# Optimization experiments

Measured on AMD Instinct MI355X. Metric: run time of the kernel, lower is better.

## Reference

```python
import jax, jax.numpy as jnp
import numpy as np

COST_CLASS = 1.0
COST_BBOX = 1.0
COST_GIOU = 1.0
ALPHA = 0.25
GAMMA = 2.0
EPS = 1e-8


def to_corners(b):
    # cxcywh -> xyxy
    cx, cy, w, h = b[..., 0], b[..., 1], b[..., 2], b[..., 3]
    return jnp.stack([cx - 0.5 * w, cy - 0.5 * h, cx + 0.5 * w, cy + 0.5 * h], axis=-1)


def generalized_iou(boxes1, boxes2):
    # boxes1: [N,4] xyxy, boxes2: [M,4] xyxy -> pairwise GIoU [N,M]
    area1 = (boxes1[:, 2] - boxes1[:, 0]) * (boxes1[:, 3] - boxes1[:, 1])  # [N]
    area2 = (boxes2[:, 2] - boxes2[:, 0]) * (boxes2[:, 3] - boxes2[:, 1])  # [M]
    lt = jnp.maximum(boxes1[:, None, :2], boxes2[None, :, :2])  # [N,M,2]
    rb = jnp.minimum(boxes1[:, None, 2:], boxes2[None, :, 2:])  # [N,M,2]
    wh = jnp.clip(rb - lt, 0.0)
    inter = wh[..., 0] * wh[..., 1]  # [N,M]
    union = area1[:, None] + area2[None, :] - inter
    iou = inter / (union + EPS)
    # smallest enclosing box
    lt_e = jnp.minimum(boxes1[:, None, :2], boxes2[None, :, :2])
    rb_e = jnp.maximum(boxes1[:, None, 2:], boxes2[None, :, 2:])
    wh_e = jnp.clip(rb_e - lt_e, 0.0)
    area_e = wh_e[..., 0] * wh_e[..., 1]
    return iou - (area_e - union) / (area_e + EPS)


def setup_inputs() -> dict:
    key = jax.random.key(0)
    k1, k2, k3, k4 = jax.random.split(key, 4)
    B, Q, C, T = 16, 900, 4, 1600
    logits = jax.random.normal(k1, (B, Q, C), dtype=jnp.float32)
    pred_bbox = jax.random.uniform(k2, (B, Q, 4), dtype=jnp.float32)
    target_bbox = jax.random.uniform(k3, (T, 4), dtype=jnp.float32)
    target_labels = jax.random.randint(k4, (T,), 0, C, dtype=jnp.int64)
    return {"logits": logits, "pred_bbox": pred_bbox,
            "target_bbox": target_bbox, "target_labels": target_labels}


def reference(logits, pred_bbox, target_bbox, target_labels):
    B, Q, C = logits.shape
    out_conf = jax.nn.sigmoid(logits.reshape(B * Q, C))  # [BQ, C]
    out_bbox = pred_bbox.reshape(B * Q, 4)
    # sigmoid focal classification cost
    neg_cost = (1.0 - ALPHA) * out_conf ** GAMMA * (-jnp.log(1.0 - out_conf + EPS))
    pos_cost = ALPHA * (1.0 - out_conf) ** GAMMA * (-jnp.log(out_conf + EPS))
    cost_class = pos_cost[:, target_labels] - neg_cost[:, target_labels]  # [BQ, T]
    # L1 cdist
    cost_bbox = jnp.sum(jnp.abs(out_bbox[:, None, :] - target_bbox[None, :, :]), axis=-1)  # [BQ, T]
    # pairwise GIoU cost
    cost_giou = -generalized_iou(to_corners(out_bbox), to_corners(target_bbox))  # [BQ, T]
    cost = COST_BBOX * cost_bbox + COST_CLASS * cost_class + COST_GIOU * cost_giou
    return cost.reshape(B, Q, -1)  # [B, Q, total_T]
```

## Files before the change

### kernel.cpp

```cpp
#include <hip/hip_runtime.h>
#include <hip/hip_bf16.h>
#include <math.h>

#define ALPHA 0.25f
#define EPS 1e-8f

__global__ __launch_bounds__(256) void class_cost_kernel(
    const float* __restrict__ logits,
    float* __restrict__ cc,
    int n)
{
    int i = blockIdx.x * 256 + threadIdx.x;
    if (i >= n) return;
    float x = logits[i];
    float p = 1.0f / (1.0f + expf(-x));
    float om = 1.0f - p;
    float pos = ALPHA * om * om * (-logf(p + EPS));
    float neg = (1.0f - ALPHA) * p * p * (-logf(om + EPS));
    cc[i] = pos - neg + 1.0f;
}

#define BQ_TILE 16

__global__ __launch_bounds__(256) void cost_kernel(
    const float* __restrict__ pred_bbox,
    const float* __restrict__ tgt_bbox,
    const int*   __restrict__ labels,
    const float* __restrict__ cc,
    float* __restrict__ out,
    int BQ, int T)
{
    int tg = blockIdx.x * 256 + threadIdx.x;
    int t0 = tg * 4;
    if (t0 >= T) return;
    int bq0 = blockIdx.y * BQ_TILE;

    float4 tb[4];
    float tx0[4], ty0[4], tx1[4], ty1[4], a2e[4];
    int lab[4];
    int4 lv = reinterpret_cast<const int4*>(labels)[tg];
    lab[0] = lv.x; lab[1] = lv.y; lab[2] = lv.z; lab[3] = lv.w;
    #pragma unroll
    for (int j = 0; j < 4; ++j) {
        tb[j] = reinterpret_cast<const float4*>(tgt_bbox)[t0 + j];
        tx0[j] = tb[j].x - 0.5f * tb[j].z;
        ty0[j] = tb[j].y - 0.5f * tb[j].w;
        tx1[j] = tb[j].x + 0.5f * tb[j].z;
        ty1[j] = tb[j].y + 0.5f * tb[j].w;
        a2e[j] = tb[j].z * tb[j].w + EPS;
    }

    #pragma unroll
    for (int i = 0; i < BQ_TILE; ++i) {
        int bq = bq0 + i;
        if (bq >= BQ) break;
        float4 pb = reinterpret_cast<const float4*>(pred_bbox)[bq];
        float4 cv = reinterpret_cast<const float4*>(cc)[bq];

        float px0 = pb.x - 0.5f * pb.z;
        float py0 = pb.y - 0.5f * pb.w;
        float px1 = pb.x + 0.5f * pb.z;
        float py1 = pb.y + 0.5f * pb.w;
        float area1 = pb.z * pb.w;

        float r[4];
        #pragma unroll
        for (int j = 0; j < 4; ++j) {
            float cls = (lab[j] == 0) ? cv.x : (lab[j] == 1) ? cv.y
                       : (lab[j] == 2) ? cv.z : cv.w;

            float l1 = (fabsf(pb.x - tb[j].x) + fabsf(pb.y - tb[j].y))
                     + (fabsf(pb.z - tb[j].z) + fabsf(pb.w - tb[j].w));

            float iwr = fminf(px1, tx1[j]) - fmaxf(px0, tx0[j]);
            float ihr = fminf(py1, ty1[j]) - fmaxf(py0, ty0[j]);
            float iw = fmaxf(iwr, 0.0f);
            float ih = fmaxf(ihr, 0.0f);
            float inter = iw * ih;

            float ew = (pb.z + tb[j].z) - iwr;
            float eh = (pb.w + tb[j].w) - ihr;
            float ae = fmaf(ew, eh, EPS);

            float u = (area1 + a2e[j]) - inter;

            float num = fmaf(inter, ae, u * u);
            float den = u * ae;
            float q = num * __builtin_amdgcn_rcpf(den);

            r[j] = (l1 + cls) - q;
        }
        float4 o = make_float4(r[0], r[1], r[2], r[3]);
        reinterpret_cast<float4*>(&out[(size_t)bq * T + t0])[0] = o;
    }
}

extern "C" void kernel_launch(void* const* d_in, const int* in_sizes, int n_in,
                              void* d_out, int out_size, void* d_ws, size_t ws_size,
                              hipStream_t stream) {
    const float* logits    = (const float*)d_in[0];
    const float* pred_bbox = (const float*)d_in[1];
    const float* tgt_bbox  = (const float*)d_in[2];
    const int*   labels    = (const int*)d_in[3];

    int BQ = in_sizes[1] / 4;
    int T  = in_sizes[3];

    float* cc = (float*)d_ws;

    int n_cc = in_sizes[0];
    class_cost_kernel<<<(n_cc + 255) / 256, 256, 0, stream>>>(logits, cc, n_cc);

    int tgroups = T / 4;
    dim3 grid((tgroups + 255) / 256, (BQ + BQ_TILE - 1) / BQ_TILE);
    cost_kernel<<<grid, 256, 0, stream>>>(pred_bbox, tgt_bbox, labels, cc,
                                          (float*)d_out, BQ, T);
}
```

Measured before the change: 124.7 us.

## Pack per-wave work units to eliminate idle lanes and precompute predicted corners

```diff
diff --git a/kernel.cpp b/kernel.cpp
--- a/kernel.cpp
+++ b/kernel.cpp
@@ -4,42 +4,66 @@
 
 #define ALPHA 0.25f
 #define EPS 1e-8f
+#define BQ_TILE 16
 
-__global__ __launch_bounds__(256) void class_cost_kernel(
+__global__ __launch_bounds__(256) void prep_kernel(
     const float* __restrict__ logits,
+    const float* __restrict__ pred_bbox,
     float* __restrict__ cc,
-    int n)
+    float4* __restrict__ pcorn,
+    int n_cc, int BQ)
 {
     int i = blockIdx.x * 256 + threadIdx.x;
-    if (i >= n) return;
-    float x = logits[i];
-    float p = 1.0f / (1.0f + expf(-x));
-    float om = 1.0f - p;
-    float pos = ALPHA * om * om * (-logf(p + EPS));
-    float neg = (1.0f - ALPHA) * p * p * (-logf(om + EPS));
-    cc[i] = pos - neg + 1.0f;
+    if (i < n_cc) {
+        float x = logits[i];
+        float p = 1.0f / (1.0f + expf(-x));
+        float om = 1.0f - p;
+        float pos = ALPHA * om * om * (-logf(p + EPS));
+        float neg = (1.0f - ALPHA) * p * p * (-logf(om + EPS));
+        cc[i] = pos - neg + 1.0f;
+    }
+    if (i < BQ) {
+        float4 pb = reinterpret_cast<const float4*>(pred_bbox)[i];
+        float4 c;
+        c.x = pb.x - 0.5f * pb.z;
+        c.y = pb.y - 0.5f * pb.w;
+        c.z = pb.x + 0.5f * pb.z;
+        c.w = pb.y + 0.5f * pb.w;
+        pcorn[i] = c;
+    }
 }
-
-#define BQ_TILE 16
 
 __global__ __launch_bounds__(256) void cost_kernel(
     const float* __restrict__ pred_bbox,
+    const float4* __restrict__ pcorn,
     const float* __restrict__ tgt_bbox,
     const int*   __restrict__ labels,
     const float* __restrict__ cc,
     float* __restrict__ out,
-    int BQ, int T)
+    int BQ, int T, int nTC, int nWU)
 {
-    int tg = blockIdx.x * 256 + threadIdx.x;
+    __shared__ float s_cc[4 * BQ_TILE * 4];
+
+    int wslot = threadIdx.x >> 6;
+    int lane  = threadIdx.x & 63;
+    int wu = blockIdx.x * 4 + wslot;
+    if (wu >= nWU) return;
+    int tc  = wu % nTC;
+    int bqt = wu / nTC;
+    int bq0 = bqt * BQ_TILE;
+
+    s_cc[wslot * 64 + lane] = cc[bq0 * 4 + lane];
+
+    int tg = tc * 64 + lane;
+    int TG = T >> 2;
+    if (tg >= TG) return;
     int t0 = tg * 4;
-    if (t0 >= T) return;
-    int bq0 = blockIdx.y * BQ_TILE;
 
     float4 tb[4];
     float tx0[4], ty0[4], tx1[4], ty1[4], a2e[4];
-    int lab[4];
+    int lidx[4];
     int4 lv = reinterpret_cast<const int4*>(labels)[tg];
-    lab[0] = lv.x; lab[1] = lv.y; lab[2] = lv.z; lab[3] = lv.w;
+    int lbl[4] = {lv.x, lv.y, lv.z, lv.w};
     #pragma unroll
     for (int j = 0; j < 4; ++j) {
         tb[j] = reinterpret_cast<const float4*>(tgt_bbox)[t0 + j];
@@ -48,32 +72,26 @@
         tx1[j] = tb[j].x + 0.5f * tb[j].z;
         ty1[j] = tb[j].y + 0.5f * tb[j].w;
         a2e[j] = tb[j].z * tb[j].w + EPS;
+        lidx[j] = wslot * 64 + lbl[j];
     }
 
     #pragma unroll
     for (int i = 0; i < BQ_TILE; ++i) {
         int bq = bq0 + i;
-        if (bq >= BQ) break;
         float4 pb = reinterpret_cast<const float4*>(pred_bbox)[bq];
-        float4 cv = reinterpret_cast<const float4*>(cc)[bq];
-
-        float px0 = pb.x - 0.5f * pb.z;
-        float py0 = pb.y - 0.5f * pb.w;
-        float px1 = pb.x + 0.5f * pb.z;
-        float py1 = pb.y + 0.5f * pb.w;
+        float4 pc = pcorn[bq];
         float area1 = pb.z * pb.w;
 
         float r[4];
         #pragma unroll
         for (int j = 0; j < 4; ++j) {
-            float cls = (lab[j] == 0) ? cv.x : (lab[j] == 1) ? cv.y
-                       : (lab[j] == 2) ? cv.z : cv.w;
+            float cls = s_cc[lidx[j] + i * 4];
 
             float l1 = (fabsf(pb.x - tb[j].x) + fabsf(pb.y - tb[j].y))
                      + (fabsf(pb.z - tb[j].z) + fabsf(pb.w - tb[j].w));
 
-            float iwr = fminf(px1, tx1[j]) - fmaxf(px0, tx0[j]);
-            float ihr = fminf(py1, ty1[j]) - fmaxf(py0, ty0[j]);
+            float iwr = fminf(pc.z, tx1[j]) - fmaxf(pc.x, tx0[j]);
+            float ihr = fminf(pc.w, ty1[j]) - fmaxf(pc.y, ty0[j]);
             float iw = fmaxf(iwr, 0.0f);
             float ih = fmaxf(ihr, 0.0f);
             float inter = iw * ih;
@@ -85,13 +103,12 @@
             float u = (area1 + a2e[j]) - inter;
 
             float num = fmaf(inter, ae, u * u);
-            float den = u * ae;
-            float q = num * __builtin_amdgcn_rcpf(den);
+            float q = num * __builtin_amdgcn_rcpf(u * ae);
 
             r[j] = (l1 + cls) - q;
         }
-        float4 o = make_float4(r[0], r[1], r[2], r[3]);
-        reinterpret_cast<float4*>(&out[(size_t)bq * T + t0])[0] = o;
+        *reinterpret_cast<float4*>(&out[(size_t)bq * T + t0]) =
+            make_float4(r[0], r[1], r[2], r[3]);
     }
 }
 
@@ -106,13 +123,19 @@
     int BQ = in_sizes[1] / 4;
     int T  = in_sizes[3];
 
-    float* cc = (float*)d_ws;
+    float*  cc    = (float*)d_ws;
+    float4* pcorn = (float4*)((char*)d_ws + (size_t)in_sizes[0] * sizeof(float));
 
     int n_cc = in_sizes[0];
-    class_cost_kernel<<<(n_cc + 255) / 256, 256, 0, stream>>>(logits, cc, n_cc);
+    int nprep = n_cc > BQ ? n_cc : BQ;
+    prep_kernel<<<(nprep + 255) / 256, 256, 0, stream>>>(
+        logits, pred_bbox, cc, pcorn, n_cc, BQ);
 
-    int tgroups = T / 4;
-    dim3 grid((tgroups + 255) / 256, (BQ + BQ_TILE - 1) / BQ_TILE);
-    cost_kernel<<<grid, 256, 0, stream>>>(pred_bbox, tgt_bbox, labels, cc,
-                                          (float*)d_out, BQ, T);
+    int TG  = T / 4;
+    int nTC = (TG + 63) / 64;
+    int nBT = BQ / BQ_TILE;
+    int nWU = nTC * nBT;
+    int blocks = (nWU + 3) / 4;
+    cost_kernel<<<blocks, 256, 0, stream>>>(pred_bbox, pcorn, tgt_bbox, labels,
+                                            cc, (float*)d_out, BQ, T, nTC, nWU);
 }
```

New measurement: 116.3 us. 1.07x faster.
